# Optimization experiments

Measured on AMD Instinct MI355X. Metric: run time of the kernel, lower is better.

The kernel has to match this reference:

```python
import jax, jax.numpy as jnp
import numpy as np

B, Q, K = 4, 512, 512
QUERY_SIZE = 512
KEY_SIZE = 512
NUM_HIDDENS = 256


def setup_inputs() -> dict:
    key = jax.random.key(0)
    k1, k2, k3, k4, k5 = jax.random.split(key, 5)
    queries = jax.random.normal(k1, (B, Q, 1, QUERY_SIZE), dtype=jnp.float32)
    keys = jax.random.normal(k2, (B, 1, K, KEY_SIZE), dtype=jnp.float32)
    # nn.Linear weights (bias=False); stored as (in, out) for einsum clarity
    W_q = jax.random.normal(k3, (QUERY_SIZE, NUM_HIDDENS), dtype=jnp.float32) * (1.0 / np.sqrt(QUERY_SIZE))
    W_k = jax.random.normal(k4, (KEY_SIZE, NUM_HIDDENS), dtype=jnp.float32) * (1.0 / np.sqrt(KEY_SIZE))
    w_v = jax.random.normal(k5, (NUM_HIDDENS,), dtype=jnp.float32) * (1.0 / np.sqrt(NUM_HIDDENS))
    return {"queries": queries, "keys": keys, "W_q": W_q, "W_k": W_k, "w_v": w_v}


def reference(queries, keys, W_q, W_k, w_v):
    # Project: queries (B,Q,1,Dq) -> (B,Q,1,H); keys (B,1,K,Dk) -> (B,1,K,H)
    q = jnp.einsum('bqod,dh->bqoh', queries, W_q)
    k = jnp.einsum('bokd,dh->bokh', keys, W_k)
    # Broadcast add -> (B,Q,K,H), tanh, reduce hidden via w_v -> (B,Q,K)
    features = jnp.tanh(q + k)
    scores = jnp.einsum('bqkh,h->bqk', features, w_v)
    return scores
```

## Files before the change

kernel.cpp:

```cpp
#include <hip/hip_runtime.h>
#include <hip/hip_bf16.h>

#define HH 256
#define DD 512
#define MM 2048
#define CSCALE 2.8853900817779268f

typedef __bf16 bf16x8 __attribute__((ext_vector_type(8)));
typedef float floatx4 __attribute__((ext_vector_type(4)));

__global__ __launch_bounds__(256) void prep_kernel(
    const float* __restrict__ Wq, const float* __restrict__ Wk,
    const float* __restrict__ wv,
    const float* __restrict__ queries, const float* __restrict__ keys,
    __bf16* __restrict__ Wt, __bf16* __restrict__ Xbf,
    float* __restrict__ wv2, float* __restrict__ sumWp)
{
  const int bx = blockIdx.x;
  if (bx < 256) {
    const int mat  = bx >> 7;
    const int tile = bx & 127;
    const int kt = tile & 15;
    const int nt = tile >> 4;
    const float* __restrict__ W = mat ? Wk : Wq;
    __bf16* __restrict__ Wo = Wt + (size_t)mat * HH * DD;
    __shared__ float lds[32][33];
    const int i = threadIdx.x >> 5;
    const int j = threadIdx.x & 31;
    const int k0 = kt * 32, n0 = nt * 32;
#pragma unroll
    for (int p = 0; p < 4; ++p)
      lds[i + p * 8][j] = W[(k0 + i + p * 8) * HH + n0 + j];
    __syncthreads();
#pragma unroll
    for (int p = 0; p < 4; ++p) {
      const int n = i + p * 8;
      Wo[(n0 + n) * DD + k0 + j] = (__bf16)(lds[j][n] * CSCALE);
    }
  } else if (bx == 256) {
    __shared__ float red[256];
    const int t = threadIdx.x;
    float w = wv[t];
    wv2[t] = -2.0f * w;
    red[t] = w;
    __syncthreads();
    for (int s = 128; s > 0; s >>= 1) {
      if (t < s) red[t] += red[t + s];
      __syncthreads();
    }
    if (t == 0) *sumWp = red[0];
  } else {
    const int blk = bx - 257;
    const size_t dst = (size_t)blk * 2048 + threadIdx.x * 8;
    const float* __restrict__ src =
        (blk < 512) ? (queries + dst) : (keys + dst - (size_t)1048576);
    float4 a = *(const float4*)(src);
    float4 b = *(const float4*)(src + 4);
    bf16x8 v;
    v[0] = (__bf16)a.x; v[1] = (__bf16)a.y; v[2] = (__bf16)a.z; v[3] = (__bf16)a.w;
    v[4] = (__bf16)b.x; v[5] = (__bf16)b.y; v[6] = (__bf16)b.z; v[7] = (__bf16)b.w;
    *(bf16x8*)(Xbf + dst) = v;
  }
}

__global__ __launch_bounds__(256, 4) void proj_kernel(
    const __bf16* __restrict__ Xbf, const __bf16* __restrict__ Wt,
    float* __restrict__ eqp, float* __restrict__ ekp)
{
  const int w    = threadIdx.x >> 6;
  const int lane = threadIdx.x & 63;
  const int quad = lane >> 4;
  const int r    = lane & 15;
  const int tw = w & 1;
  const int ks = w >> 1;
  const bool is_k = (blockIdx.z != 0);
  const __bf16* __restrict__ X  = Xbf + (is_k ? (size_t)1048576 : 0);
  const __bf16* __restrict__ Wb = Wt + (is_k ? (size_t)HH * DD : 0);

  const int m0 = blockIdx.x * 32 + tw * 16;
  const int n0 = blockIdx.y * 32;

  floatx4 acc0 = {0.f, 0.f, 0.f, 0.f};
  floatx4 acc1 = {0.f, 0.f, 0.f, 0.f};
  const __bf16* arow = X + (size_t)(m0 + r) * DD + ks * 256 + quad * 8;
  const __bf16* b0   = Wb + (size_t)(n0 + r) * DD + ks * 256 + quad * 8;
  const __bf16* b1   = b0 + 16 * DD;

#pragma unroll
  for (int kk = 0; kk < 256; kk += 32) {
    bf16x8 af  = *(const bf16x8*)(arow + kk);
    bf16x8 bf0 = *(const bf16x8*)(b0 + kk);
    bf16x8 bf1 = *(const bf16x8*)(b1 + kk);
    acc0 = __builtin_amdgcn_mfma_f32_16x16x32_bf16(af, bf0, acc0, 0, 0, 0);
    acc1 = __builtin_amdgcn_mfma_f32_16x16x32_bf16(af, bf1, acc1, 0, 0, 0);
  }

  __shared__ float part[2][64][9];
  if (ks == 1) {
#pragma unroll
    for (int i = 0; i < 4; ++i) {
      part[tw][lane][i]     = acc0[i];
      part[tw][lane][4 + i] = acc1[i];
    }
  }
  __syncthreads();
  if (ks == 0) {
#pragma unroll
    for (int i = 0; i < 4; ++i) {
      acc0[i] += part[tw][lane][i];
      acc1[i] += part[tw][lane][4 + i];
    }
    const int mrow = m0 + quad * 4;
    if (!is_k) {
#pragma unroll
      for (int i = 0; i < 4; ++i) {
        eqp[(size_t)(mrow + i) * HH + n0 + r] =
            __builtin_amdgcn_exp2f(acc0[i]);
        eqp[(size_t)(mrow + i) * HH + n0 + 16 + r] =
            __builtin_amdgcn_exp2f(acc1[i]);
      }
    } else {
      const int na = n0 + r, nb = n0 + 16 + r;
#pragma unroll
      for (int i = 0; i < 4; ++i) {
        ekp[((size_t)(na >> 2) * MM + (mrow + i)) * 4 + (na & 3)] =
            __builtin_amdgcn_exp2f(acc0[i]);
        ekp[((size_t)(nb >> 2) * MM + (mrow + i)) * 4 + (nb & 3)] =
            __builtin_amdgcn_exp2f(acc1[i]);
      }
    }
  }
}

__global__ __launch_bounds__(256, 4) void score_kernel(
    const float* __restrict__ eqp, const float4* __restrict__ ekp,
    const float* __restrict__ wv2, const float* __restrict__ sumWp,
    float* __restrict__ out)
{
  const int t  = threadIdx.x;
  const int b  = blockIdx.z;
  const int k  = blockIdx.x * 256 + t;
  const int q0 = blockIdx.y * 4;
  const float sumW = *sumWp;

  const float4* __restrict__ kptr = ekp + (size_t)b * 512 + k;
  const float* __restrict__ qb = eqp + (size_t)(b * 512 + q0) * HH;

  float acc[4] = {0.f, 0.f, 0.f, 0.f};

#pragma unroll 4
  for (int hq = 0; hq < 64; ++hq) {
    float4 ek4 = kptr[(size_t)hq * MM];
    const float* wq = wv2 + hq * 4;
    float w0 = wq[0], w1 = wq[1], w2 = wq[2], w3 = wq[3];
#pragma unroll
    for (int qi = 0; qi < 4; ++qi) {
      const float* eqr = qb + qi * HH + hq * 4;
      float e0 = eqr[0], e1 = eqr[1], e2 = eqr[2], e3 = eqr[3];
      float u0 = fmaf(e0, ek4.x, 1.0f);
      float u1 = fmaf(e1, ek4.y, 1.0f);
      float u2 = fmaf(e2, ek4.z, 1.0f);
      float u3 = fmaf(e3, ek4.w, 1.0f);
      float n02 = fmaf(w2, u0, w0 * u2);
      float n13 = fmaf(w3, u1, w1 * u3);
      float r02 = __builtin_amdgcn_rcpf(u0 * u2);
      float r13 = __builtin_amdgcn_rcpf(u1 * u3);
      acc[qi] = fmaf(n02, r02, acc[qi]);
      acc[qi] = fmaf(n13, r13, acc[qi]);
    }
  }

  const size_t ob = ((size_t)(b * 512 + q0)) * 512 + blockIdx.x * 256 + t;
  out[ob]        = sumW + acc[0];
  out[ob + 512]  = sumW + acc[1];
  out[ob + 1024] = sumW + acc[2];
  out[ob + 1536] = sumW + acc[3];
}

extern "C" void kernel_launch(void* const* d_in, const int* in_sizes, int n_in,
                              void* d_out, int out_size, void* d_ws, size_t ws_size,
                              hipStream_t stream) {
  (void)in_sizes; (void)n_in; (void)out_size; (void)ws_size;
  const float* queries = (const float*)d_in[0];
  const float* Keys    = (const float*)d_in[1];
  const float* Wq      = (const float*)d_in[2];
  const float* Wk      = (const float*)d_in[3];
  const float* wv      = (const float*)d_in[4];
  float* out = (float*)d_out;

  char* ws = (char*)d_ws;
  __bf16* Wt    = (__bf16*)ws;
  float*  wv2   = (float*)(ws + (512 << 10));
  float*  sumWp = (float*)(ws + (513 << 10));
  __bf16* Xbf   = (__bf16*)(ws + (1 << 20));
  float*  eqp   = (float*)(ws + (5ull << 20));
  float*  ekp   = (float*)(ws + (7ull << 20));

  prep_kernel<<<dim3(1281), 256, 0, stream>>>(
      Wq, Wk, wv, queries, Keys, Wt, Xbf, wv2, sumWp);
  proj_kernel<<<dim3(64, 8, 2), 256, 0, stream>>>(Xbf, Wt, eqp, ekp);
  score_kernel<<<dim3(2, 128, 4), 256, 0, stream>>>(
      eqp, (const float4*)ekp, wv2, sumWp, out);
}
```

Before: 118.2 us.

## Combine four tanh terms per reciprocal and halve queries per score block

The score kernel now merges four hidden units into one fraction, so it needs one reciprocal per four terms instead of one per two. This cuts transcendental-unit work, but adds a few multiplies and a larger product that could overflow or lose precision. Each block now handles 2 queries instead of 4, doubling the grid and dropping the occupancy hint from launch bounds. The smaller block means each loaded key vector is reused across fewer queries, so key traffic rises in exchange for more parallelism.

```diff
diff --git a/kernel.cpp b/kernel.cpp
--- a/kernel.cpp
+++ b/kernel.cpp
@@ -132,7 +132,24 @@
   }
 }
 
-__global__ __launch_bounds__(256, 4) void score_kernel(
+__device__ __forceinline__ float quad_term(
+    float4 ek4, const float* __restrict__ eqr,
+    float w0, float w1, float w2, float w3, float acc)
+{
+  float u0 = fmaf(eqr[0], ek4.x, 1.0f);
+  float u1 = fmaf(eqr[1], ek4.y, 1.0f);
+  float u2 = fmaf(eqr[2], ek4.z, 1.0f);
+  float u3 = fmaf(eqr[3], ek4.w, 1.0f);
+  float p01 = u0 * u1;
+  float p23 = u2 * u3;
+  float n01 = fmaf(w1, u0, w0 * u1);
+  float n23 = fmaf(w3, u2, w2 * u3);
+  float N   = fmaf(n23, p01, n01 * p23);
+  float r   = __builtin_amdgcn_rcpf(p01 * p23);
+  return fmaf(N, r, acc);
+}
+
+__global__ __launch_bounds__(256) void score_kernel(
     const float* __restrict__ eqp, const float4* __restrict__ ekp,
     const float* __restrict__ wv2, const float* __restrict__ sumWp,
     float* __restrict__ out)
@@ -140,41 +157,26 @@
   const int t  = threadIdx.x;
   const int b  = blockIdx.z;
   const int k  = blockIdx.x * 256 + t;
-  const int q0 = blockIdx.y * 4;
+  const int q0 = blockIdx.y * 2;
   const float sumW = *sumWp;
 
   const float4* __restrict__ kptr = ekp + (size_t)b * 512 + k;
   const float* __restrict__ qb = eqp + (size_t)(b * 512 + q0) * HH;
 
-  float acc[4] = {0.f, 0.f, 0.f, 0.f};
+  float acc0 = 0.f, acc1 = 0.f;
 
 #pragma unroll 4
   for (int hq = 0; hq < 64; ++hq) {
     float4 ek4 = kptr[(size_t)hq * MM];
     const float* wq = wv2 + hq * 4;
     float w0 = wq[0], w1 = wq[1], w2 = wq[2], w3 = wq[3];
-#pragma unroll
-    for (int qi = 0; qi < 4; ++qi) {
-      const float* eqr = qb + qi * HH + hq * 4;
-      float e0 = eqr[0], e1 = eqr[1], e2 = eqr[2], e3 = eqr[3];
-      float u0 = fmaf(e0, ek4.x, 1.0f);
-      float u1 = fmaf(e1, ek4.y, 1.0f);
-      float u2 = fmaf(e2, ek4.z, 1.0f);
-      float u3 = fmaf(e3, ek4.w, 1.0f);
-      float n02 = fmaf(w2, u0, w0 * u2);
-      float n13 = fmaf(w3, u1, w1 * u3);
-      float r02 = __builtin_amdgcn_rcpf(u0 * u2);
-      float r13 = __builtin_amdgcn_rcpf(u1 * u3);
-      acc[qi] = fmaf(n02, r02, acc[qi]);
-      acc[qi] = fmaf(n13, r13, acc[qi]);
-    }
+    acc0 = quad_term(ek4, qb + hq * 4,      w0, w1, w2, w3, acc0);
+    acc1 = quad_term(ek4, qb + HH + hq * 4, w0, w1, w2, w3, acc1);
   }
 
   const size_t ob = ((size_t)(b * 512 + q0)) * 512 + blockIdx.x * 256 + t;
-  out[ob]        = sumW + acc[0];
-  out[ob + 512]  = sumW + acc[1];
-  out[ob + 1024] = sumW + acc[2];
-  out[ob + 1536] = sumW + acc[3];
+  out[ob]       = sumW + acc0;
+  out[ob + 512] = sumW + acc1;
 }
 
 extern "C" void kernel_launch(void* const* d_in, const int* in_sizes, int n_in,
@@ -199,6 +201,6 @@
   prep_kernel<<<dim3(1281), 256, 0, stream>>>(
       Wq, Wk, wv, queries, Keys, Wt, Xbf, wv2, sumWp);
   proj_kernel<<<dim3(64, 8, 2), 256, 0, stream>>>(Xbf, Wt, eqp, ekp);
-  score_kernel<<<dim3(2, 128, 4), 256, 0, stream>>>(
+  score_kernel<<<dim3(2, 256, 4), 256, 0, stream>>>(
       eqp, (const float4*)ekp, wv2, sumWp, out);
 }
```

After: 114.2 us. 1.04x faster.
